# Kernel optimization log

Measured on AMD Instinct MI355X. Metric: run time of the kernel, lower is better.

Reference implementation:

```python
import jax, jax.numpy as jnp
import numpy as np

N, NFEAT, NHID, NREL, NCLASS, NHEADS = 4096, 512, 64, 64, 16, 8
ALPHA = 0.2   # LeakyReLU negative slope
NEG = -9e15   # pyGAT mask value


def _gat_layer(x, rel, mask, adj_ad, W, a1, a2, concat):
    # x: [N, Fin], rel: [nrel, Fin], mask: [N, N] bool, adj_ad: [N, nrel]
    xr = x + adj_ad @ rel                 # relation-augmented node features
    h = xr @ W                            # [N, Fout]
    f1 = h @ a1                           # [N]  (a^T[Wh_i||Wh_j] = f1_i + f2_j)
    f2 = h @ a2                           # [N]
    e = jax.nn.leaky_relu(f1[:, None] + f2[None, :], ALPHA)  # [N, N]
    att = jax.nn.softmax(jnp.where(mask, e, NEG), axis=1)
    out = att @ h                         # [N, Fout]
    return jax.nn.elu(out) if concat else out


def setup_inputs() -> dict:
    key = jax.random.key(0)
    ks = jax.random.split(key, 12)
    x = jax.random.normal(ks[0], (N, NFEAT), jnp.float32)
    rel = jax.random.normal(ks[1], (NREL, NFEAT), jnp.float32)
    rel_dict = jax.random.randint(ks[2], (N,), 0, NREL, jnp.int32)
    adj = (jax.random.uniform(ks[3], (N, N)) < 0.01).astype(jnp.float32)
    adj = jnp.maximum(adj, jnp.eye(N, dtype=jnp.float32))  # self loops
    adj_ad = jax.random.uniform(ks[4], (N, NREL), jnp.float32)
    adj_ad = adj_ad / adj_ad.sum(axis=1, keepdims=True)
    s_in = 1.0 / np.sqrt(NFEAT)
    s_hid = 1.0 / np.sqrt(NHID)
    s_cat = 1.0 / np.sqrt(NHID * NHEADS)
    W_heads = jax.random.normal(ks[5], (NHEADS, NFEAT, NHID), jnp.float32) * s_in
    a1_heads = jax.random.normal(ks[6], (NHEADS, NHID), jnp.float32) * s_hid
    a2_heads = jax.random.normal(ks[7], (NHEADS, NHID), jnp.float32) * s_hid
    W_out = jax.random.normal(ks[8], (NHID * NHEADS, NFEAT), jnp.float32) * s_cat
    a1_out = jax.random.normal(ks[9], (NFEAT,), jnp.float32) * s_in
    a2_out = jax.random.normal(ks[10], (NFEAT,), jnp.float32) * s_in
    lin_W = jax.random.normal(ks[11], (NFEAT, NCLASS), jnp.float32) * s_in
    lin_b = jnp.zeros((NCLASS,), jnp.float32)
    return {"x": x, "rel": rel, "rel_dict": rel_dict, "adj": adj, "adj_ad": adj_ad,
            "W_heads": W_heads, "a1_heads": a1_heads, "a2_heads": a2_heads,
            "W_out": W_out, "a1_out": a1_out, "a2_out": a2_out,
            "lin_W": lin_W, "lin_b": lin_b}


def reference(x, rel, rel_dict, adj, adj_ad, W_heads, a1_heads, a2_heads,
              W_out, a1_out, a2_out, lin_W, lin_b):
    # dropout is identity at inference (training=False); rel_dict is only used
    # by the repo to build adj/adj_ad, so it is a non-math constant here.
    mask = adj > 0
    # multi-head GAT layer, heads fused via vmap then concatenated on feature dim
    heads = jax.vmap(lambda W, a1, a2: _gat_layer(x, rel, mask, adj_ad, W, a1, a2, True))(
        W_heads, a1_heads, a2_heads)                      # [H, N, NHID]
    hcat = jnp.moveaxis(heads, 0, 1).reshape(N, NHEADS * NHID)  # [N, H*NHID]
    h2 = _gat_layer(hcat, rel, mask, adj_ad, W_out, a1_out, a2_out, False)  # [N, NFEAT]
    logits = jax.nn.elu(h2 @ lin_W + lin_b)               # [N, NCLASS]
    return jax.nn.log_softmax(logits, axis=1)
```

## Files before the change

kernel.cpp:

```cpp
#include <hip/hip_runtime.h>

#define NN      4096
#define FEAT    512
#define NHID    64
#define NHEADS  8
#define NCLS    16
#define MAXDEG  128
#define ALPHA   0.2f

typedef __bf16 bf16_t;
typedef __bf16 bf16x8_t __attribute__((ext_vector_type(8)));
typedef float  f32x4_t  __attribute__((ext_vector_type(4)));
typedef unsigned short us8_t __attribute__((ext_vector_type(8)));

__device__ inline unsigned short f2bf(float f) {
    unsigned int u = __float_as_uint(f);
    u += 0x7fffu + ((u >> 16) & 1u);
    return (unsigned short)(u >> 16);
}
__device__ inline float bfu2f(unsigned short b) {
    return __uint_as_float(((unsigned int)b) << 16);
}

#define NB_CSR   512
#define NB_RMM   2048
#define NB_WPERM 2052

__global__ __launch_bounds__(256) void prep_kernel(
    const float* __restrict__ adj, int* __restrict__ deg, int* __restrict__ cols,
    const float* __restrict__ adj_ad, const float* __restrict__ rel,
    const float* __restrict__ x, float* __restrict__ R, bf16_t* __restrict__ Abf,
    const float* __restrict__ Wh, const float* __restrict__ Wo,
    unsigned short* __restrict__ WcT, unsigned short* __restrict__ WoT,
    float* __restrict__ f1o, float* __restrict__ f2o) {
    int b = blockIdx.x;
    int t = threadIdx.x;
    __shared__ float sa[2][64];
    if (b < NB_CSR) {
        int wid  = b * 4 + (t >> 6);
        int lane = t & 63;
        for (int row = wid; row < NN; row += 2048) {
            const float4* r4 = (const float4*)(adj + (size_t)row * NN);
            float4 v[16];
            #pragma unroll
            for (int q = 0; q < 16; ++q) v[q] = r4[lane + 64 * q];
            unsigned long long mask = 0ULL;
            #pragma unroll
            for (int q = 0; q < 16; ++q) {
                mask |= (unsigned long long)(v[q].x > 0.0f) << (4 * q);
                mask |= (unsigned long long)(v[q].y > 0.0f) << (4 * q + 1);
                mask |= (unsigned long long)(v[q].z > 0.0f) << (4 * q + 2);
                mask |= (unsigned long long)(v[q].w > 0.0f) << (4 * q + 3);
            }
            int c = __popcll(mask);
            int pre = c;
            #pragma unroll
            for (int off = 1; off < 64; off <<= 1) {
                int n = __shfl_up(pre, off);
                if (lane >= off) pre += n;
            }
            int tot  = __shfl(pre, 63);
            int base = pre - c;
            int* colrow = cols + row * MAXDEG;
            unsigned long long mm = mask;
            int idx = base;
            while (mm) {
                int bit = __ffsll((unsigned long long)mm) - 1;
                mm &= mm - 1;
                int j = 4 * (lane + 64 * (bit >> 2)) + (bit & 3);
                if (idx < MAXDEG) colrow[idx] = j;
                ++idx;
            }
            if (lane == 0) deg[row] = tot > MAXDEG ? MAXDEG : tot;
        }
    } else if (b < NB_CSR + NB_RMM) {
        int half = t >> 7;
        int tt = t & 127;
        int i = (b - NB_CSR) * 2 + half;
        if (tt < 64) sa[half][tt] = adj_ad[i * 64 + tt];
        __syncthreads();
        float4 acc = make_float4(0.f, 0.f, 0.f, 0.f);
        #pragma unroll 4
        for (int r = 0; r < 64; ++r) {
            float a = sa[half][r];
            float4 rv = ((const float4*)(rel + r * FEAT))[tt];
            acc.x += a * rv.x; acc.y += a * rv.y;
            acc.z += a * rv.z; acc.w += a * rv.w;
        }
        ((float4*)(R + (size_t)i * FEAT))[tt] = acc;
        float4 xv = ((const float4*)(x + (size_t)i * FEAT))[tt];
        ushort4 o;
        o.x = f2bf(acc.x + xv.x); o.y = f2bf(acc.y + xv.y);
        o.z = f2bf(acc.z + xv.z); o.w = f2bf(acc.w + xv.w);
        *(ushort4*)(Abf + (size_t)i * FEAT + 4 * tt) = o;
    } else {
        int gid = (b - NB_CSR - NB_RMM) * 256 + t;
        if (gid < 262144) {
            int idx = gid;
            int n = idx >> 9, k = idx & 511;
            int h = n >> 6, f = n & 63;
            WcT[idx] = f2bf(Wh[(h * 512 + k) * 64 + f]);
        } else if (gid < 524288) {
            int idx = gid - 262144;
            int n = idx >> 9, k = idx & 511;
            WoT[idx] = f2bf(Wo[k * 512 + n]);
        } else {
            int idx = gid - 524288;
            ((float4*)f1o)[idx] = make_float4(0.f, 0.f, 0.f, 0.f);
            ((float4*)f2o)[idx] = make_float4(0.f, 0.f, 0.f, 0.f);
        }
    }
}

__global__ __launch_bounds__(256) void gemm_bf16_dot_kernel(
    const bf16_t* __restrict__ A, const bf16_t* __restrict__ Bt,
    unsigned short* __restrict__ Cbf,
    const float* __restrict__ a1, const float* __restrict__ a2,
    float* __restrict__ f1, float* __restrict__ f2, int layer2) {
    __shared__ __align__(16) bf16_t As[64][72];
    __shared__ __align__(16) bf16_t Bs[64][72];
    const int bm = blockIdx.x * 64;
    const int bn = blockIdx.y * 64;
    const int t  = threadIdx.x;
    const int lr = t >> 3;
    const int lc = (t & 7) * 8;
    const int l  = t & 63;
    const int w  = t >> 6;
    const int mrow = w * 16 + (l & 15);
    const int nrow = l & 15;
    const int q8 = (l >> 4) * 8;

    const bf16_t* Ap0 = A  + (size_t)(bm + lr)      * FEAT + lc;
    const bf16_t* Ap1 = A  + (size_t)(bm + 32 + lr) * FEAT + lc;
    const bf16_t* Bp0 = Bt + (size_t)(bn + lr)      * FEAT + lc;
    const bf16_t* Bp1 = Bt + (size_t)(bn + 32 + lr) * FEAT + lc;
    uint4 ra0 = *(const uint4*)(Ap0);
    uint4 ra1 = *(const uint4*)(Ap1);
    uint4 rb0 = *(const uint4*)(Bp0);
    uint4 rb1 = *(const uint4*)(Bp1);

    f32x4_t acc[4] = {};
    for (int k0 = 0; k0 < FEAT; k0 += 64) {
        *(uint4*)&As[lr][lc]      = ra0;
        *(uint4*)&As[32 + lr][lc] = ra1;
        *(uint4*)&Bs[lr][lc]      = rb0;
        *(uint4*)&Bs[32 + lr][lc] = rb1;
        __syncthreads();
        if (k0 + 64 < FEAT) {
            ra0 = *(const uint4*)(Ap0 + k0 + 64);
            ra1 = *(const uint4*)(Ap1 + k0 + 64);
            rb0 = *(const uint4*)(Bp0 + k0 + 64);
            rb1 = *(const uint4*)(Bp1 + k0 + 64);
        }
        #pragma unroll
        for (int kk = 0; kk < 64; kk += 32) {
            bf16x8_t a = *(const bf16x8_t*)&As[mrow][kk + q8];
            #pragma unroll
            for (int nt = 0; nt < 4; ++nt) {
                bf16x8_t b = *(const bf16x8_t*)&Bs[nt * 16 + nrow][kk + q8];
                acc[nt] = __builtin_amdgcn_mfma_f32_16x16x32_bf16(a, b, acc[nt], 0, 0, 0);
            }
        }
        __syncthreads();
    }
    const int crow = bm + w * 16 + (l >> 4) * 4;
    const int ccol = bn + (l & 15);
    #pragma unroll
    for (int nt = 0; nt < 4; ++nt)
        #pragma unroll
        for (int r = 0; r < 4; ++r)
            Cbf[(size_t)(crow + r) * FEAT + ccol + nt * 16] = f2bf(acc[nt][r]);

    float a1v[4], a2v[4];
    #pragma unroll
    for (int nt = 0; nt < 4; ++nt) {
        a1v[nt] = a1[bn + (l & 15) + nt * 16];
        a2v[nt] = a2[bn + (l & 15) + nt * 16];
    }
    float p1[4] = {}, p2[4] = {};
    #pragma unroll
    for (int nt = 0; nt < 4; ++nt)
        #pragma unroll
        for (int r = 0; r < 4; ++r) {
            p1[r] += acc[nt][r] * a1v[nt];
            p2[r] += acc[nt][r] * a2v[nt];
        }
    #pragma unroll
    for (int off = 1; off <= 8; off <<= 1)
        #pragma unroll
        for (int r = 0; r < 4; ++r) {
            p1[r] += __shfl_xor(p1[r], off);
            p2[r] += __shfl_xor(p2[r], off);
        }
    if ((l & 15) == 0) {
        int row = bm + w * 16 + (l >> 4) * 4;
        if (layer2) {
            #pragma unroll
            for (int r = 0; r < 4; ++r) {
                atomicAdd(&f1[row + r], p1[r]);
                atomicAdd(&f2[row + r], p2[r]);
            }
        } else {
            #pragma unroll
            for (int r = 0; r < 4; ++r) {
                f1[blockIdx.y * NN + row + r] = p1[r];
                f2[blockIdx.y * NN + row + r] = p2[r];
            }
        }
    }
}

__global__ __launch_bounds__(512) void att1_kernel(
    const bf16_t* __restrict__ Hbf, const float* __restrict__ f1,
    const float* __restrict__ f2, const int* __restrict__ deg,
    const int* __restrict__ cols, const float* __restrict__ R,
    bf16_t* __restrict__ outbf) {
    int i = blockIdx.x;
    int tid = threadIdx.x;
    int h = tid >> 6;
    int l = tid & 63;
    __shared__ int jl[MAXDEG];
    __shared__ float se[NHEADS][MAXDEG];
    __shared__ float part[NHEADS][FEAT];
    __shared__ float sinv[NHEADS];
    __shared__ int sdeg;
    if (tid == 0) sdeg = deg[i];
    __syncthreads();
    int d = sdeg;
    int dpad = (d + 31) & ~31;
    for (int k = tid; k < dpad; k += 512)
        jl[k] = (k < d) ? cols[i * MAXDEG + k] : i;
    __syncthreads();
    float fi = f1[h * NN + i];
    float lmax = -1e30f;
    for (int k = l; k < d; k += 64) {
        float e = fi + f2[h * NN + jl[k]];
        e = e > 0.0f ? e : ALPHA * e;
        se[h][k] = e;
        lmax = fmaxf(lmax, e);
    }
    for (int off = 32; off; off >>= 1) lmax = fmaxf(lmax, __shfl_down(lmax, off));
    float m = __shfl(lmax, 0);
    float ls = 0.0f;
    for (int k = l; k < d; k += 64) {
        float p = __expf(se[h][k] - m);
        se[h][k] = p;
        ls += p;
    }
    for (int k = d + l; k < dpad; k += 64) se[h][k] = 0.0f;
    for (int off = 32; off; off >>= 1) ls += __shfl_down(ls, off);
    if (l == 0) sinv[h] = 1.0f / ls;
    __syncthreads();
    const int myhead = l >> 3;
    float acc[8] = {};
    for (int k0 = 0; k0 < dpad; k0 += 32) {
        float pw[4];
        const bf16_t* rp[4];
        #pragma unroll
        for (int j = 0; j < 4; ++j) {
            int k = k0 + j * 8 + h;
            pw[j] = se[myhead][k];
            rp[j] = Hbf + (size_t)jl[k] * FEAT + l * 8;
        }
        #pragma unroll
        for (int j = 0; j < 4; ++j) {
            us8_t v = *(const us8_t*)rp[j];
            float p = pw[j];
            #pragma unroll
            for (int q = 0; q < 8; ++q) acc[q] += p * bfu2f(v[q]);
        }
    }
    *(float4*)&part[h][l * 8]     = make_float4(acc[0], acc[1], acc[2], acc[3]);
    *(float4*)&part[h][l * 8 + 4] = make_float4(acc[4], acc[5], acc[6], acc[7]);
    __syncthreads();
    {
        float sum = 0.0f;
        #pragma unroll
        for (int w2 = 0; w2 < NHEADS; ++w2) sum += part[w2][tid];
        float o = sum * sinv[tid >> 6];
        o = o > 0.0f ? o : __expf(o) - 1.0f;
        o += R[(size_t)i * FEAT + tid];
        ((unsigned short*)outbf)[(size_t)i * FEAT + tid] = f2bf(o);
    }
}

__global__ __launch_bounds__(256) void att2_final_kernel(
    const bf16_t* __restrict__ Hbf, const float* __restrict__ f1,
    const float* __restrict__ f2, const int* __restrict__ deg,
    const int* __restrict__ cols, const float* __restrict__ linW,
    const float* __restrict__ linb, float* __restrict__ out) {
    int i = blockIdx.x;
    int t = threadIdx.x;
    __shared__ int jl[MAXDEG];
    __shared__ float sp[MAXDEG];
    __shared__ float red[4];
    __shared__ float part[3][FEAT];
    __shared__ float hrow[FEAT];
    __shared__ float clsred[16][NCLS];
    __shared__ float sl[NCLS];
    __shared__ int sdeg;
    if (t == 0) sdeg = deg[i];
    __syncthreads();
    int d = sdeg;
    int dpad = (d + 15) & ~15;
    if (t < dpad) jl[t] = (t < d) ? cols[i * MAXDEG + t] : i;
    __syncthreads();
    float e = 0.0f, lmax = -1e30f;
    if (t < d) {
        e = f1[i] + f2[jl[t]];
        e = e > 0.0f ? e : ALPHA * e;
        lmax = e;
    }
    for (int off = 32; off; off >>= 1) lmax = fmaxf(lmax, __shfl_down(lmax, off));
    if ((t & 63) == 0) red[t >> 6] = lmax;
    __syncthreads();
    float m = fmaxf(fmaxf(red[0], red[1]), fmaxf(red[2], red[3]));
    float p = 0.0f;
    if (t < d) p = __expf(e - m);
    if (t < dpad) sp[t] = p;
    float ls = p;
    for (int off = 32; off; off >>= 1) ls += __shfl_down(ls, off);
    __syncthreads();
    if ((t & 63) == 0) red[t >> 6] = ls;
    __syncthreads();
    float s = red[0] + red[1] + red[2] + red[3];
    float inv = 1.0f / s;
    const int slot = t >> 6;
    const int cg   = t & 63;
    float acc[8] = {};
    for (int k0 = 0; k0 < dpad; k0 += 16) {
        float pw[4];
        const bf16_t* rp[4];
        #pragma unroll
        for (int j = 0; j < 4; ++j) {
            int k = k0 + j * 4 + slot;
            pw[j] = sp[k];
            rp[j] = Hbf + (size_t)jl[k] * FEAT + cg * 8;
        }
        #pragma unroll
        for (int j = 0; j < 4; ++j) {
            us8_t v = *(const us8_t*)rp[j];
            float pk = pw[j];
            #pragma unroll
            for (int q = 0; q < 8; ++q) acc[q] += pk * bfu2f(v[q]);
        }
    }
    if (slot > 0) {
        float* dst = &part[slot - 1][cg * 8];
        *(float4*)(dst)     = make_float4(acc[0], acc[1], acc[2], acc[3]);
        *(float4*)(dst + 4) = make_float4(acc[4], acc[5], acc[6], acc[7]);
    }
    __syncthreads();
    if (slot == 0) {
        #pragma unroll
        for (int sl2 = 0; sl2 < 3; ++sl2)
            #pragma unroll
            for (int j = 0; j < 8; ++j) acc[j] += part[sl2][cg * 8 + j];
        float* dst = &hrow[cg * 8];
        *(float4*)(dst)     = make_float4(acc[0] * inv, acc[1] * inv, acc[2] * inv, acc[3] * inv);
        *(float4*)(dst + 4) = make_float4(acc[4] * inv, acc[5] * inv, acc[6] * inv, acc[7] * inv);
    }
    __syncthreads();
    {
        int c = t & 15;
        int seg = t >> 4;
        float partial = 0.0f;
        int f0 = seg * 32;
        #pragma unroll 8
        for (int f = f0; f < f0 + 32; ++f) partial += hrow[f] * linW[f * NCLS + c];
        clsred[seg][c] = partial;
    }
    __syncthreads();
    if (t < NCLS) {
        float logit = linb[t];
        #pragma unroll
        for (int seg = 0; seg < 16; ++seg) logit += clsred[seg][t];
        logit = logit > 0.0f ? logit : __expf(logit) - 1.0f;
        sl[t] = logit;
    }
    __syncthreads();
    if (t < NCLS) {
        float mm = sl[0];
        #pragma unroll
        for (int c = 1; c < NCLS; ++c) mm = fmaxf(mm, sl[c]);
        float ssum = 0.0f;
        #pragma unroll
        for (int c = 0; c < NCLS; ++c) ssum += __expf(sl[c] - mm);
        out[i * NCLS + t] = sl[t] - mm - logf(ssum);
    }
}

extern "C" void kernel_launch(void* const* d_in, const int* in_sizes, int n_in,
                              void* d_out, int out_size, void* d_ws, size_t ws_size,
                              hipStream_t stream) {
    const float* x        = (const float*)d_in[0];
    const float* rel      = (const float*)d_in[1];
    const float* adj      = (const float*)d_in[3];
    const float* adj_ad   = (const float*)d_in[4];
    const float* W_heads  = (const float*)d_in[5];
    const float* a1_heads = (const float*)d_in[6];
    const float* a2_heads = (const float*)d_in[7];
    const float* W_out    = (const float*)d_in[8];
    const float* a1_out   = (const float*)d_in[9];
    const float* a2_out   = (const float*)d_in[10];
    const float* lin_W    = (const float*)d_in[11];
    const float* lin_b    = (const float*)d_in[12];
    float* out = (float*)d_out;

    char* ws = (char*)d_ws;
    bf16_t* Abf  = (bf16_t*)(ws);
    bf16_t* Abf2 = (bf16_t*)(ws + (4u  << 20));
    bf16_t* Hbf1 = (bf16_t*)(ws + (8u  << 20));
    bf16_t* Hbf2 = (bf16_t*)(ws + (12u << 20));
    float*  R    = (float*) (ws + (16u << 20));
    bf16_t* WcT  = (bf16_t*)(ws + (24u << 20));
    bf16_t* WoT  = (bf16_t*)(ws + (24u << 20) + (512u << 10));
    float*  f1   = (float*) (ws + (25u << 20));
    float*  f2   = (float*) (ws + (25u << 20) + (128u << 10));
    float*  f1o  = (float*) (ws + (25u << 20) + (256u << 10));
    float*  f2o  = (float*) (ws + (25u << 20) + (272u << 10));
    int*    deg  = (int*)   (ws + (25u << 20) + (288u << 10));
    int*    cols = (int*)   (ws + (26u << 20));

    prep_kernel<<<NB_CSR + NB_RMM + NB_WPERM, 256, 0, stream>>>(
        adj, deg, cols, adj_ad, rel, x, R, Abf,
        W_heads, W_out, (unsigned short*)WcT, (unsigned short*)WoT, f1o, f2o);
    gemm_bf16_dot_kernel<<<dim3(64, 8), 256, 0, stream>>>(
        Abf, WcT, (unsigned short*)Hbf1, a1_heads, a2_heads, f1, f2, 0);
    att1_kernel<<<NN, 512, 0, stream>>>(Hbf1, f1, f2, deg, cols, R, Abf2);
    gemm_bf16_dot_kernel<<<dim3(64, 8), 256, 0, stream>>>(
        Abf2, WoT, (unsigned short*)Hbf2, a1_out, a2_out, f1o, f2o, 1);
    att2_final_kernel<<<NN, 256, 0, stream>>>(Hbf2, f1o, f2o, deg, cols, lin_W, lin_b, out);
}
```

Measured before the change: 201.7 us.

## Split adjacency CSR build into bitmap pass and compaction fused into GEMM

The prep kernel now only streams the dense adjacency into a compact bitmap, one block per row with fully coalesced loads. The column-list compaction (prefix scan, ffs loop) moves into an extra grid row of the first GEMM launch, so it runs alongside the GEMM tiles. This is meant to spread the 64 MB adjacency read across more blocks and take the serial compaction off the critical path. The cost is an extra bitmap buffer in the workspace and a heterogeneous GEMM grid, whose compaction blocks may run longer than the GEMM tiles.

```diff
diff --git a/kernel.cpp b/kernel.cpp
--- a/kernel.cpp
+++ b/kernel.cpp
@@ -22,12 +22,8 @@
     return __uint_as_float(((unsigned int)b) << 16);
 }
 
-#define NB_CSR   512
-#define NB_RMM   2048
-#define NB_WPERM 2052
-
 __global__ __launch_bounds__(256) void prep_kernel(
-    const float* __restrict__ adj, int* __restrict__ deg, int* __restrict__ cols,
+    const float* __restrict__ adj, unsigned short* __restrict__ bitmap,
     const float* __restrict__ adj_ad, const float* __restrict__ rel,
     const float* __restrict__ x, float* __restrict__ R, bf16_t* __restrict__ Abf,
     const float* __restrict__ Wh, const float* __restrict__ Wo,
@@ -36,47 +32,23 @@
     int b = blockIdx.x;
     int t = threadIdx.x;
     __shared__ float sa[2][64];
-    if (b < NB_CSR) {
-        int wid  = b * 4 + (t >> 6);
-        int lane = t & 63;
-        for (int row = wid; row < NN; row += 2048) {
-            const float4* r4 = (const float4*)(adj + (size_t)row * NN);
-            float4 v[16];
-            #pragma unroll
-            for (int q = 0; q < 16; ++q) v[q] = r4[lane + 64 * q];
-            unsigned long long mask = 0ULL;
-            #pragma unroll
-            for (int q = 0; q < 16; ++q) {
-                mask |= (unsigned long long)(v[q].x > 0.0f) << (4 * q);
-                mask |= (unsigned long long)(v[q].y > 0.0f) << (4 * q + 1);
-                mask |= (unsigned long long)(v[q].z > 0.0f) << (4 * q + 2);
-                mask |= (unsigned long long)(v[q].w > 0.0f) << (4 * q + 3);
-            }
-            int c = __popcll(mask);
-            int pre = c;
-            #pragma unroll
-            for (int off = 1; off < 64; off <<= 1) {
-                int n = __shfl_up(pre, off);
-                if (lane >= off) pre += n;
-            }
-            int tot  = __shfl(pre, 63);
-            int base = pre - c;
-            int* colrow = cols + row * MAXDEG;
-            unsigned long long mm = mask;
-            int idx = base;
-            while (mm) {
-                int bit = __ffsll((unsigned long long)mm) - 1;
-                mm &= mm - 1;
-                int j = 4 * (lane + 64 * (bit >> 2)) + (bit & 3);
-                if (idx < MAXDEG) colrow[idx] = j;
-                ++idx;
-            }
-            if (lane == 0) deg[row] = tot > MAXDEG ? MAXDEG : tot;
-        }
-    } else if (b < NB_CSR + NB_RMM) {
+    if (b < NN) {
+        const float4* r4 = (const float4*)(adj + (size_t)b * NN) + 4 * t;
+        float4 v0 = r4[0], v1 = r4[1], v2 = r4[2], v3 = r4[3];
+        unsigned m = 0;
+        m |= (v0.x > 0.0f) << 0;  m |= (v0.y > 0.0f) << 1;
+        m |= (v0.z > 0.0f) << 2;  m |= (v0.w > 0.0f) << 3;
+        m |= (v1.x > 0.0f) << 4;  m |= (v1.y > 0.0f) << 5;
+        m |= (v1.z > 0.0f) << 6;  m |= (v1.w > 0.0f) << 7;
+        m |= (v2.x > 0.0f) << 8;  m |= (v2.y > 0.0f) << 9;
+        m |= (v2.z > 0.0f) << 10; m |= (v2.w > 0.0f) << 11;
+        m |= (v3.x > 0.0f) << 12; m |= (v3.y > 0.0f) << 13;
+        m |= (v3.z > 0.0f) << 14; m |= (v3.w > 0.0f) << 15;
+        bitmap[b * 256 + t] = (unsigned short)m;
+    } else if (b < NN + 2048) {
         int half = t >> 7;
         int tt = t & 127;
-        int i = (b - NB_CSR) * 2 + half;
+        int i = (b - NN) * 2 + half;
         if (tt < 64) sa[half][tt] = adj_ad[i * 64 + tt];
         __syncthreads();
         float4 acc = make_float4(0.f, 0.f, 0.f, 0.f);
@@ -94,7 +66,7 @@
         o.z = f2bf(acc.z + xv.z); o.w = f2bf(acc.w + xv.w);
         *(ushort4*)(Abf + (size_t)i * FEAT + 4 * tt) = o;
     } else {
-        int gid = (b - NB_CSR - NB_RMM) * 256 + t;
+        int gid = (b - NN - 2048) * 256 + t;
         if (gid < 262144) {
             int idx = gid;
             int n = idx >> 9, k = idx & 511;
@@ -116,7 +88,39 @@
     const bf16_t* __restrict__ A, const bf16_t* __restrict__ Bt,
     unsigned short* __restrict__ Cbf,
     const float* __restrict__ a1, const float* __restrict__ a2,
-    float* __restrict__ f1, float* __restrict__ f2, int layer2) {
+    float* __restrict__ f1, float* __restrict__ f2, int layer2,
+    const unsigned long long* __restrict__ bm64,
+    int* __restrict__ deg, int* __restrict__ cols) {
+    if (blockIdx.y == 8) {
+        int wv = threadIdx.x >> 6, lane = threadIdx.x & 63;
+        int row0 = blockIdx.x * 64 + wv * 16;
+        unsigned long long w64 = bm64[(size_t)row0 * 64 + lane];
+        for (int rr = 0; rr < 16; ++rr) {
+            int row = row0 + rr;
+            unsigned long long nxt = (rr < 15)
+                ? bm64[(size_t)(row + 1) * 64 + lane] : 0ULL;
+            int c = __popcll(w64);
+            int pre = c;
+            #pragma unroll
+            for (int off = 1; off < 64; off <<= 1) {
+                int n = __shfl_up(pre, off);
+                if (lane >= off) pre += n;
+            }
+            int tot  = __shfl(pre, 63);
+            int idx  = pre - c;
+            int* colrow = cols + row * MAXDEG;
+            unsigned long long mm = w64;
+            while (mm) {
+                int bit = __ffsll(mm) - 1;
+                mm &= mm - 1;
+                if (idx < MAXDEG) colrow[idx] = 64 * lane + bit;
+                ++idx;
+            }
+            if (lane == 0) deg[row] = tot > MAXDEG ? MAXDEG : tot;
+            w64 = nxt;
+        }
+        return;
+    }
     __shared__ __align__(16) bf16_t As[64][72];
     __shared__ __align__(16) bf16_t Bs[64][72];
     const int bm = blockIdx.x * 64;
@@ -421,14 +425,17 @@
     float*  f2o  = (float*) (ws + (25u << 20) + (272u << 10));
     int*    deg  = (int*)   (ws + (25u << 20) + (288u << 10));
     int*    cols = (int*)   (ws + (26u << 20));
-
-    prep_kernel<<<NB_CSR + NB_RMM + NB_WPERM, 256, 0, stream>>>(
-        adj, deg, cols, adj_ad, rel, x, R, Abf,
+    unsigned short* bitmap = (unsigned short*)(ws + (28u << 20));
+
+    prep_kernel<<<NN + 2048 + 2052, 256, 0, stream>>>(
+        adj, bitmap, adj_ad, rel, x, R, Abf,
         W_heads, W_out, (unsigned short*)WcT, (unsigned short*)WoT, f1o, f2o);
-    gemm_bf16_dot_kernel<<<dim3(64, 8), 256, 0, stream>>>(
-        Abf, WcT, (unsigned short*)Hbf1, a1_heads, a2_heads, f1, f2, 0);
+    gemm_bf16_dot_kernel<<<dim3(64, 9), 256, 0, stream>>>(
+        Abf, WcT, (unsigned short*)Hbf1, a1_heads, a2_heads, f1, f2, 0,
+        (const unsigned long long*)bitmap, deg, cols);
     att1_kernel<<<NN, 512, 0, stream>>>(Hbf1, f1, f2, deg, cols, R, Abf2);
     gemm_bf16_dot_kernel<<<dim3(64, 8), 256, 0, stream>>>(
-        Abf2, WoT, (unsigned short*)Hbf2, a1_out, a2_out, f1o, f2o, 1);
+        Abf2, WoT, (unsigned short*)Hbf2, a1_out, a2_out, f1o, f2o, 1,
+        (const unsigned long long*)bitmap, deg, cols);
     att2_final_kernel<<<NN, 256, 0, stream>>>(Hbf2, f1o, f2o, deg, cols, lin_W, lin_b, out);
 }
```

Measured after the change: 208.0 us. 1.03x slower.
